# Kernel optimization log

Measured on AMD Instinct MI355X. Metric: run time of the kernel, lower is better.

## Reference

```python
import jax, jax.numpy as jnp
import numpy as np

D_MODEL = 512
N_HEADS = 8
HEAD_DIM = 64
INNER = N_HEADS * HEAD_DIM
PAD = 128  # flash-attention style tile padding used by the custom kernel


def setup_inputs() -> dict:
    key = jax.random.key(0)
    ks = jax.random.split(key, 5)
    B, S = 2, 2048
    scale = 0.02
    return {
        "hidden_states": jax.random.normal(ks[0], (B, S, D_MODEL), dtype=jnp.float32),
        "Wq": jax.random.normal(ks[1], (D_MODEL, INNER), dtype=jnp.float32) * scale,
        "Wk": jax.random.normal(ks[2], (D_MODEL, INNER), dtype=jnp.float32) * scale,
        "Wv": jax.random.normal(ks[3], (D_MODEL, INNER), dtype=jnp.float32) * scale,
        "Wo": jax.random.normal(ks[4], (INNER, D_MODEL), dtype=jnp.float32) * scale,
    }


def _padded_attention(q, k, v):
    """Emulates torch.ops.knl.fwd: pad seq to a multiple of PAD, run
    non-causal scaled dot-product attention masking padded keys, then
    slice back to the original length. q,k,v: [B, S, INNER]."""
    B, S, _ = q.shape
    pad_len = (-S) % PAD
    Sp = S + pad_len
    pad_cfg = ((0, 0), (0, pad_len), (0, 0))
    qp = jnp.pad(q, pad_cfg)
    kp = jnp.pad(k, pad_cfg)
    vp = jnp.pad(v, pad_cfg)
    # [B, H, Sp, hd]
    qh = qp.reshape(B, Sp, N_HEADS, HEAD_DIM).transpose(0, 2, 1, 3)
    kh = kp.reshape(B, Sp, N_HEADS, HEAD_DIM).transpose(0, 2, 1, 3)
    vh = vp.reshape(B, Sp, N_HEADS, HEAD_DIM).transpose(0, 2, 1, 3)
    scale = 1.0 / np.sqrt(HEAD_DIM).astype(np.float32)
    scores = jnp.einsum("bhqd,bhkd->bhqk", qh, kh) * scale  # [B,H,Sp,Sp]
    key_valid = jnp.arange(Sp) < S  # mask out padded keys
    scores = jnp.where(key_valid[None, None, None, :], scores, jnp.float32(-1e30))
    probs = jax.nn.softmax(scores, axis=-1)
    out = jnp.einsum("bhqk,bhkd->bhqd", probs, vh)  # [B,H,Sp,hd]
    out = out.transpose(0, 2, 1, 3).reshape(B, Sp, INNER)
    return out[:, :S, :]


def reference(hidden_states, Wq, Wk, Wv, Wo):
    q = hidden_states @ Wq
    k = hidden_states @ Wk
    v = hidden_states @ Wv
    attn = _padded_attention(q, k, v)
    return attn @ Wo
```

## Files before the change

kernel.cpp:

```cpp
#include <hip/hip_runtime.h>

using bf16 = __bf16;
using bf16x4 = __attribute__((ext_vector_type(4))) __bf16;
using bf16x8 = __attribute__((ext_vector_type(8))) __bf16;
using floatx4 = __attribute__((ext_vector_type(4))) float;
using half4 = __attribute__((ext_vector_type(4))) _Float16;
using half8 = __attribute__((ext_vector_type(8))) _Float16;

#define D_MODEL 512
#define S_LEN 2048
#define HD 64
#define NH 8
#define M_TOT 4096
#define RS 72
#define NSPLIT 4
#define KSPAN (S_LEN / NSPLIT)
#define QSCALE 0.18033688f

__device__ __forceinline__ bf16x8 ld8(const bf16* p) {
    return *reinterpret_cast<const bf16x8*>(p);
}
__device__ __forceinline__ void gl_lds16(const bf16* g, bf16* l) {
    __builtin_amdgcn_global_load_lds(
        (const __attribute__((address_space(1))) void*)g,
        (__attribute__((address_space(3))) void*)l, 16, 0, 0);
}

__global__ __launch_bounds__(256) void prep(const float* __restrict__ w0,
                                            const float* __restrict__ w1,
                                            const float* __restrict__ w2,
                                            const float* __restrict__ w3,
                                            const float* __restrict__ X,
                                            bf16* __restrict__ WT,
                                            bf16* __restrict__ Xb) {
    int z = blockIdx.z;
    if (z == 4) {
        int i = (blockIdx.x * 256 + threadIdx.x) * 8;
        float4 a = *reinterpret_cast<const float4*>(X + i);
        float4 b = *reinterpret_cast<const float4*>(X + i + 4);
        bf16x8 o;
        o[0] = (bf16)a.x; o[1] = (bf16)a.y; o[2] = (bf16)a.z; o[3] = (bf16)a.w;
        o[4] = (bf16)b.x; o[5] = (bf16)b.y; o[6] = (bf16)b.z; o[7] = (bf16)b.w;
        *reinterpret_cast<bf16x8*>(Xb + i) = o;
        return;
    }
    if (blockIdx.x >= 256) return;
    __shared__ float t[32][33];
    const float* in = z == 0 ? w0 : z == 1 ? w1 : z == 2 ? w2 : w3;
    bf16* o = WT + (size_t)z * D_MODEL * D_MODEL;
    int x = threadIdx.x & 31;
    int y = threadIdx.x >> 5;
    int k0 = (blockIdx.x & 15) * 32, n0 = (blockIdx.x >> 4) * 32;
    for (int r = y; r < 32; r += 8) t[r][x] = in[(size_t)(k0 + r) * D_MODEL + n0 + x];
    __syncthreads();
    for (int r = y; r < 32; r += 8) o[(size_t)(n0 + r) * D_MODEL + k0 + x] = (bf16)t[x][r];
}

__global__ __launch_bounds__(256) void gemm_qkvf(const bf16* __restrict__ X,
                                                 const bf16* __restrict__ WT,
                                                 bf16* __restrict__ qk,
                                                 bf16* __restrict__ VT) {
    __shared__ __align__(16) bf16 As[64 * 64];
    __shared__ __align__(16) bf16 Bs[64 * 64];
    int lane = threadIdx.x & 63, wave = threadIdx.x >> 6;
    int l15 = lane & 15, quad = lane >> 4;
    int m0 = blockIdx.x * 64;
    int n0 = blockIdx.y * 64;
    int z = n0 >> 9;
    int h = (n0 >> 6) & 7;
    int wm = (wave & 1) * 32, wn = (wave >> 1) * 32;
    float oscale = (z == 0) ? QSCALE : 1.0f;

    int sr = lane >> 3;
    int sc = (lane & 7) ^ sr;
    const bf16* gA = X  + (size_t)(m0 + wave * 16 + sr) * D_MODEL + sc * 8;
    const bf16* gB = WT + (size_t)(n0 + wave * 16 + sr) * D_MODEL + sc * 8;
    bf16* ldsA = &As[(wave * 16) * 64];
    bf16* ldsB = &Bs[(wave * 16) * 64];
    int rx = l15 & 7;

    floatx4 acc[2][2] = {};
    for (int k0 = 0; k0 < D_MODEL; k0 += 64) {
        __syncthreads();
        gl_lds16(gA + k0, ldsA);
        gl_lds16(gA + (size_t)8 * D_MODEL + k0, ldsA + 8 * 64);
        gl_lds16(gB + k0, ldsB);
        gl_lds16(gB + (size_t)8 * D_MODEL + k0, ldsB + 8 * 64);
        __syncthreads();
        bf16x8 af[2][2], bfr[2][2];
        #pragma unroll
        for (int mt = 0; mt < 2; mt++)
            #pragma unroll
            for (int kh = 0; kh < 2; kh++)
                af[mt][kh] = ld8(&As[(wm + mt * 16 + l15) * 64 + (((quad + 4 * kh) ^ rx)) * 8]);
        #pragma unroll
        for (int nt = 0; nt < 2; nt++)
            #pragma unroll
            for (int kh = 0; kh < 2; kh++)
                bfr[nt][kh] = ld8(&Bs[(wn + nt * 16 + l15) * 64 + (((quad + 4 * kh) ^ rx)) * 8]);
        #pragma unroll
        for (int mt = 0; mt < 2; mt++)
            #pragma unroll
            for (int nt = 0; nt < 2; nt++) {
                acc[mt][nt] = __builtin_amdgcn_mfma_f32_16x16x32_bf16(af[mt][0], bfr[nt][0], acc[mt][nt], 0, 0, 0);
                acc[mt][nt] = __builtin_amdgcn_mfma_f32_16x16x32_bf16(af[mt][1], bfr[nt][1], acc[mt][nt], 0, 0, 0);
            }
    }

    if (z < 2) {
        bf16* dst = qk + (size_t)z * M_TOT * HD * NH;
        #pragma unroll
        for (int mt = 0; mt < 2; mt++)
            #pragma unroll
            for (int nt = 0; nt < 2; nt++)
                #pragma unroll
                for (int r = 0; r < 4; r++) {
                    int m = m0 + wm + mt * 16 + quad * 4 + r;
                    int n = wn + nt * 16 + l15;
                    int b = m >> 11, s = m & 2047;
                    dst[((size_t)(b * NH + h) * S_LEN + s) * HD + n] = (bf16)(acc[mt][nt][r] * oscale);
                }
    } else {
        #pragma unroll
        for (int mt = 0; mt < 2; mt++)
            #pragma unroll
            for (int nt = 0; nt < 2; nt++) {
                int m = m0 + wm + mt * 16 + quad * 4;
                int d = wn + nt * 16 + l15;
                int b = m >> 11, s = m & 2047;
                bf16x4 pk;
                pk[0] = (bf16)acc[mt][nt][0]; pk[1] = (bf16)acc[mt][nt][1];
                pk[2] = (bf16)acc[mt][nt][2]; pk[3] = (bf16)acc[mt][nt][3];
                *reinterpret_cast<bf16x4*>(&VT[((size_t)(b * NH + h) * HD + d) * S_LEN + s]) = pk;
            }
    }
}

__global__ __launch_bounds__(256) void attn_split(const bf16* __restrict__ qg,
                                                  const bf16* __restrict__ kg,
                                                  const bf16* __restrict__ vt,
                                                  _Float16* __restrict__ Opart,
                                                  float* __restrict__ lsum) {
    __shared__ __align__(16) bf16 Kl[64 * 64];
    __shared__ __align__(16) bf16 Vl[64 * 64];
    __shared__ __align__(16) bf16 Pl[128 * RS];
    int tid = threadIdx.x;
    int lane = tid & 63, wave = tid >> 6;
    int l15 = lane & 15, quad = lane >> 4;
    int bh = blockIdx.y, split = blockIdx.z;
    int q0 = blockIdx.x * 128;
    const bf16* qb = qg + (size_t)bh * S_LEN * HD;
    const bf16* kb = kg + (size_t)bh * S_LEN * HD + (size_t)split * KSPAN * HD;
    const bf16* vb = vt + (size_t)bh * HD * S_LEN + split * KSPAN;

    int qA = q0 + wave * 32 + l15;
    int qB = qA + 16;
    bf16x8 qf[2][2];
    qf[0][0] = ld8(qb + (size_t)qA * HD + quad * 8);
    qf[0][1] = ld8(qb + (size_t)qA * HD + 32 + quad * 8);
    qf[1][0] = ld8(qb + (size_t)qB * HD + quad * 8);
    qf[1][1] = ld8(qb + (size_t)qB * HD + 32 + quad * 8);
    floatx4 O[2][4] = {};
    float l_i[2] = {0.f, 0.f};

    int sr = lane >> 3;
    int sc = (lane & 7) ^ sr;
    const bf16* gK = kb + (size_t)(wave * 16 + sr) * HD + sc * 8;
    const bf16* gV = vb + (size_t)(wave * 16 + sr) * S_LEN + sc * 8;
    bf16* ldsK = &Kl[(wave * 16) * 64];
    bf16* ldsV = &Vl[(wave * 16) * 64];
    int rx = l15 & 7;

    for (int kt = 0; kt < KSPAN; kt += 64) {
        __syncthreads();
        gl_lds16(gK + (size_t)kt * HD, ldsK);
        gl_lds16(gK + (size_t)(kt + 8) * HD, ldsK + 8 * 64);
        gl_lds16(gV + kt, ldsV);
        gl_lds16(gV + (size_t)8 * S_LEN + kt, ldsV + 8 * 64);
        __syncthreads();

        #pragma unroll
        for (int qh = 0; qh < 2; qh++) {
            floatx4 sc4[4];
            #pragma unroll
            for (int nt = 0; nt < 4; nt++) {
                floatx4 z = {};
                bf16x8 a0 = ld8(&Kl[(nt * 16 + l15) * 64 + (quad ^ rx) * 8]);
                bf16x8 a1 = ld8(&Kl[(nt * 16 + l15) * 64 + ((quad + 4) ^ rx) * 8]);
                z = __builtin_amdgcn_mfma_f32_16x16x32_bf16(a0, qf[qh][0], z, 0, 0, 0);
                z = __builtin_amdgcn_mfma_f32_16x16x32_bf16(a1, qf[qh][1], z, 0, 0, 0);
                sc4[nt] = z;
            }
            #pragma unroll
            for (int nt = 0; nt < 4; nt++) {
                bf16x4 pk;
                #pragma unroll
                for (int r = 0; r < 4; r++) {
                    float p = exp2f(sc4[nt][r]);
                    l_i[qh] += p;
                    pk[r] = (bf16)p;
                }
                *reinterpret_cast<bf16x4*>(
                    &Pl[(wave * 32 + qh * 16 + l15) * RS + nt * 16 + quad * 4]) = pk;
            }
        }
        __syncthreads();

        bf16x8 pb[2][2];
        #pragma unroll
        for (int qh = 0; qh < 2; qh++) {
            pb[qh][0] = ld8(&Pl[(wave * 32 + qh * 16 + l15) * RS + quad * 8]);
            pb[qh][1] = ld8(&Pl[(wave * 32 + qh * 16 + l15) * RS + 32 + quad * 8]);
        }
        #pragma unroll
        for (int nt = 0; nt < 4; nt++) {
            bf16x8 v0 = ld8(&Vl[(nt * 16 + l15) * 64 + (quad ^ rx) * 8]);
            bf16x8 v1 = ld8(&Vl[(nt * 16 + l15) * 64 + ((quad + 4) ^ rx) * 8]);
            #pragma unroll
            for (int qh = 0; qh < 2; qh++) {
                O[qh][nt] = __builtin_amdgcn_mfma_f32_16x16x32_bf16(v0, pb[qh][0], O[qh][nt], 0, 0, 0);
                O[qh][nt] = __builtin_amdgcn_mfma_f32_16x16x32_bf16(v1, pb[qh][1], O[qh][nt], 0, 0, 0);
            }
        }
    }

    #pragma unroll
    for (int qh = 0; qh < 2; qh++) {
        float l = l_i[qh];
        l += __shfl_xor(l, 16, 64);
        l += __shfl_xor(l, 32, 64);
        int q = (qh == 0) ? qA : qB;
        size_t obase = (((size_t)(split * 16 + bh)) * S_LEN + q) * HD;
        #pragma unroll
        for (int nt = 0; nt < 4; nt++) {
            half4 h;
            h[0] = (_Float16)O[qh][nt][0]; h[1] = (_Float16)O[qh][nt][1];
            h[2] = (_Float16)O[qh][nt][2]; h[3] = (_Float16)O[qh][nt][3];
            *reinterpret_cast<half4*>(&Opart[obase + nt * 16 + quad * 4]) = h;
        }
        if (quad == 0)
            lsum[((size_t)(split * 16 + bh)) * S_LEN + q] = l;
    }
}

__global__ __launch_bounds__(256) void gemm_outm(const _Float16* __restrict__ Opart,
                                                 const float* __restrict__ lsum,
                                                 const bf16* __restrict__ WoT,
                                                 float* __restrict__ out) {
    __shared__ __align__(16) bf16 As[64 * 64];
    __shared__ __align__(16) bf16 Bs[64 * 64];
    __shared__ float invl[64 * 8];
    int tid = threadIdx.x;
    int lane = tid & 63, wave = tid >> 6;
    int l15 = lane & 15, quad = lane >> 4;
    int m0 = blockIdx.x * 64;
    int n0 = blockIdx.y * 64;
    int wm = (wave & 1) * 32, wn = (wave >> 1) * 32;

    for (int i = tid; i < 512; i += 256) {
        int row = i >> 3, h = i & 7;
        int mm = m0 + row;
        int b = mm >> 11, q = mm & 2047;
        float l = 0.f;
        #pragma unroll
        for (int s = 0; s < NSPLIT; s++)
            l += lsum[((size_t)(s * 16 + b * NH + h)) * S_LEN + q];
        invl[i] = 1.f / l;
    }

    int sr = lane >> 3;
    int sc = (lane & 7) ^ sr;
    const bf16* gB = WoT + (size_t)(n0 + wave * 16 + sr) * D_MODEL + sc * 8;
    bf16* ldsA = &As[(wave * 16) * 64];
    bf16* ldsB = &Bs[(wave * 16) * 64];
    int rx = l15 & 7;

    floatx4 acc[2][2] = {};
    for (int k0 = 0; k0 < D_MODEL; k0 += 64) {
        __syncthreads();
        gl_lds16(gB + k0, ldsB);
        gl_lds16(gB + (size_t)8 * D_MODEL + k0, ldsB + 8 * 64);
        int h = k0 >> 6;
        #pragma unroll
        for (int st = 0; st < 2; st++) {
            int row = wave * 16 + sr + st * 8;
            int mm = m0 + row;
            int b = mm >> 11, q = mm & 2047;
            float iv = invl[row * 8 + h];
            float a8[8] = {};
            #pragma unroll
            for (int s = 0; s < NSPLIT; s++) {
                half8 hp = *reinterpret_cast<const half8*>(
                    &Opart[(((size_t)(s * 16 + b * NH + h)) * S_LEN + q) * HD + sc * 8]);
                #pragma unroll
                for (int j = 0; j < 8; j++) a8[j] += (float)hp[j];
            }
            bf16x8 v;
            #pragma unroll
            for (int j = 0; j < 8; j++) v[j] = (bf16)(a8[j] * iv);
            *reinterpret_cast<bf16x8*>(ldsA + st * 512 + lane * 8) = v;
        }
        __syncthreads();
        bf16x8 af[2][2], bfr[2][2];
        #pragma unroll
        for (int mt = 0; mt < 2; mt++)
            #pragma unroll
            for (int kh = 0; kh < 2; kh++)
                af[mt][kh] = ld8(&As[(wm + mt * 16 + l15) * 64 + (((quad + 4 * kh) ^ rx)) * 8]);
        #pragma unroll
        for (int nt = 0; nt < 2; nt++)
            #pragma unroll
            for (int kh = 0; kh < 2; kh++)
                bfr[nt][kh] = ld8(&Bs[(wn + nt * 16 + l15) * 64 + (((quad + 4 * kh) ^ rx)) * 8]);
        #pragma unroll
        for (int mt = 0; mt < 2; mt++)
            #pragma unroll
            for (int nt = 0; nt < 2; nt++) {
                acc[mt][nt] = __builtin_amdgcn_mfma_f32_16x16x32_bf16(af[mt][0], bfr[nt][0], acc[mt][nt], 0, 0, 0);
                acc[mt][nt] = __builtin_amdgcn_mfma_f32_16x16x32_bf16(af[mt][1], bfr[nt][1], acc[mt][nt], 0, 0, 0);
            }
    }

    #pragma unroll
    for (int mt = 0; mt < 2; mt++)
        #pragma unroll
        for (int nt = 0; nt < 2; nt++)
            #pragma unroll
            for (int r = 0; r < 4; r++) {
                int m = m0 + wm + mt * 16 + quad * 4 + r;
                int n = n0 + wn + nt * 16 + l15;
                out[(size_t)m * D_MODEL + n] = acc[mt][nt][r];
            }
}

extern "C" void kernel_launch(void* const* d_in, const int* in_sizes, int n_in,
                              void* d_out, int out_size, void* d_ws, size_t ws_size,
                              hipStream_t stream) {
    const float* X  = (const float*)d_in[0];
    const float* Wq = (const float*)d_in[1];
    const float* Wk = (const float*)d_in[2];
    const float* Wv = (const float*)d_in[3];
    const float* Wo = (const float*)d_in[4];
    float* out = (float*)d_out;
    bf16* ws  = (bf16*)d_ws;

    bf16* Xb  = ws;
    bf16* WT  = Xb + (size_t)M_TOT * D_MODEL;
    bf16* qk  = WT + (size_t)4 * D_MODEL * D_MODEL;
    bf16* VT  = qk + (size_t)2 * M_TOT * D_MODEL;
    _Float16* Opart = (_Float16*)(VT + (size_t)M_TOT * D_MODEL);
    float* lbuf = (float*)(Opart + (size_t)NSPLIT * 16 * S_LEN * HD);

    prep<<<dim3(1024, 1, 5), 256, 0, stream>>>(Wq, Wk, Wv, Wo, X, WT, Xb);
    gemm_qkvf<<<dim3(64, 24), 256, 0, stream>>>(Xb, WT, qk, VT);
    attn_split<<<dim3(16, 16, NSPLIT), 256, 0, stream>>>(qk,
                                                         qk + (size_t)M_TOT * D_MODEL,
                                                         VT, Opart, lbuf);
    gemm_outm<<<dim3(64, 8), 256, 0, stream>>>(Opart, lbuf,
                                               WT + (size_t)3 * D_MODEL * D_MODEL, out);
}
```

Measured before the change: 132.7 us.

## Pass attention probabilities via lane shuffles instead of LDS, halve query tile

The P matrix is no longer written to a shared-memory staging buffer and read back after a barrier. It is rearranged from the score accumulator layout into the MFMA operand layout with cross-lane shuffles and selects. Each block now handles 64 queries, one 16-row tile per wave, and the grid doubles. The launch bound asks for higher occupancy. This removes an LDS round-trip and a __syncthreads per tile, but it halves K/V reuse per block, so K/V tiles are loaded twice as often, and it adds many shuffle instructions.

```diff
diff --git a/kernel.cpp b/kernel.cpp
--- a/kernel.cpp
+++ b/kernel.cpp
@@ -12,7 +12,6 @@
 #define HD 64
 #define NH 8
 #define M_TOT 4096
-#define RS 72
 #define NSPLIT 4
 #define KSPAN (S_LEN / NSPLIT)
 #define QSCALE 0.18033688f
@@ -136,32 +135,26 @@
     }
 }
 
-__global__ __launch_bounds__(256) void attn_split(const bf16* __restrict__ qg,
-                                                  const bf16* __restrict__ kg,
-                                                  const bf16* __restrict__ vt,
-                                                  _Float16* __restrict__ Opart,
-                                                  float* __restrict__ lsum) {
+__global__ __launch_bounds__(256, 8) void attn_split(const bf16* __restrict__ qg,
+                                                     const bf16* __restrict__ kg,
+                                                     const bf16* __restrict__ vt,
+                                                     _Float16* __restrict__ Opart,
+                                                     float* __restrict__ lsum) {
     __shared__ __align__(16) bf16 Kl[64 * 64];
     __shared__ __align__(16) bf16 Vl[64 * 64];
-    __shared__ __align__(16) bf16 Pl[128 * RS];
     int tid = threadIdx.x;
     int lane = tid & 63, wave = tid >> 6;
     int l15 = lane & 15, quad = lane >> 4;
     int bh = blockIdx.y, split = blockIdx.z;
-    int q0 = blockIdx.x * 128;
+    int q0 = blockIdx.x * 64;
     const bf16* qb = qg + (size_t)bh * S_LEN * HD;
     const bf16* kb = kg + (size_t)bh * S_LEN * HD + (size_t)split * KSPAN * HD;
     const bf16* vb = vt + (size_t)bh * HD * S_LEN + split * KSPAN;
-
-    int qA = q0 + wave * 32 + l15;
-    int qB = qA + 16;
-    bf16x8 qf[2][2];
-    qf[0][0] = ld8(qb + (size_t)qA * HD + quad * 8);
-    qf[0][1] = ld8(qb + (size_t)qA * HD + 32 + quad * 8);
-    qf[1][0] = ld8(qb + (size_t)qB * HD + quad * 8);
-    qf[1][1] = ld8(qb + (size_t)qB * HD + 32 + quad * 8);
-    floatx4 O[2][4] = {};
-    float l_i[2] = {0.f, 0.f};
+    int q = q0 + wave * 16 + l15;
+    bf16x8 qf0 = ld8(qb + (size_t)q * HD + quad * 8);
+    bf16x8 qf1 = ld8(qb + (size_t)q * HD + 32 + quad * 8);
+    floatx4 O[4] = {};
+    float l_i = 0.f;
 
     int sr = lane >> 3;
     int sc = (lane & 7) ^ sr;
@@ -170,6 +163,9 @@
     bf16* ldsK = &Kl[(wave * 16) * 64];
     bf16* ldsV = &Vl[(wave * 16) * 64];
     int rx = l15 & 7;
+    int sa = ((quad & 1) << 5) + l15;
+    int sb = sa + 16;
+    bool himux = (quad & 2) != 0;
 
     for (int kt = 0; kt < KSPAN; kt += 64) {
         __syncthreads();
@@ -179,68 +175,71 @@
         gl_lds16(gV + (size_t)8 * S_LEN + kt, ldsV + 8 * 64);
         __syncthreads();
 
-        #pragma unroll
-        for (int qh = 0; qh < 2; qh++) {
-            floatx4 sc4[4];
-            #pragma unroll
-            for (int nt = 0; nt < 4; nt++) {
-                floatx4 z = {};
-                bf16x8 a0 = ld8(&Kl[(nt * 16 + l15) * 64 + (quad ^ rx) * 8]);
-                bf16x8 a1 = ld8(&Kl[(nt * 16 + l15) * 64 + ((quad + 4) ^ rx) * 8]);
-                z = __builtin_amdgcn_mfma_f32_16x16x32_bf16(a0, qf[qh][0], z, 0, 0, 0);
-                z = __builtin_amdgcn_mfma_f32_16x16x32_bf16(a1, qf[qh][1], z, 0, 0, 0);
-                sc4[nt] = z;
-            }
-            #pragma unroll
-            for (int nt = 0; nt < 4; nt++) {
-                bf16x4 pk;
-                #pragma unroll
-                for (int r = 0; r < 4; r++) {
-                    float p = exp2f(sc4[nt][r]);
-                    l_i[qh] += p;
-                    pk[r] = (bf16)p;
-                }
-                *reinterpret_cast<bf16x4*>(
-                    &Pl[(wave * 32 + qh * 16 + l15) * RS + nt * 16 + quad * 4]) = pk;
-            }
-        }
-        __syncthreads();
-
-        bf16x8 pb[2][2];
-        #pragma unroll
-        for (int qh = 0; qh < 2; qh++) {
-            pb[qh][0] = ld8(&Pl[(wave * 32 + qh * 16 + l15) * RS + quad * 8]);
-            pb[qh][1] = ld8(&Pl[(wave * 32 + qh * 16 + l15) * RS + 32 + quad * 8]);
-        }
+        floatx4 sc4[4];
+        #pragma unroll
+        for (int nt = 0; nt < 4; nt++) {
+            floatx4 z = {};
+            bf16x8 a0 = ld8(&Kl[(nt * 16 + l15) * 64 + (quad ^ rx) * 8]);
+            bf16x8 a1 = ld8(&Kl[(nt * 16 + l15) * 64 + ((quad + 4) ^ rx) * 8]);
+            z = __builtin_amdgcn_mfma_f32_16x16x32_bf16(a0, qf0, z, 0, 0, 0);
+            z = __builtin_amdgcn_mfma_f32_16x16x32_bf16(a1, qf1, z, 0, 0, 0);
+            sc4[nt] = z;
+        }
+
+        int2 pq[4];
+        #pragma unroll
+        for (int nt = 0; nt < 4; nt++) {
+            bf16x4 pk;
+            #pragma unroll
+            for (int r = 0; r < 4; r++) {
+                float p = exp2f(sc4[nt][r]);
+                l_i += p;
+                pk[r] = (bf16)p;
+            }
+            pq[nt] = __builtin_bit_cast(int2, pk);
+        }
+
+        bf16x8 pb[2];
+        #pragma unroll
+        for (int h2 = 0; h2 < 2; h2++) {
+            int t0 = __shfl(pq[2 * h2].x,     sa, 64);
+            int t1 = __shfl(pq[2 * h2].y,     sa, 64);
+            int t2 = __shfl(pq[2 * h2 + 1].x, sa, 64);
+            int t3 = __shfl(pq[2 * h2 + 1].y, sa, 64);
+            int u0 = __shfl(pq[2 * h2].x,     sb, 64);
+            int u1 = __shfl(pq[2 * h2].y,     sb, 64);
+            int u2 = __shfl(pq[2 * h2 + 1].x, sb, 64);
+            int u3 = __shfl(pq[2 * h2 + 1].y, sb, 64);
+            int4 v;
+            v.x = himux ? t2 : t0;
+            v.y = himux ? t3 : t1;
+            v.z = himux ? u2 : u0;
+            v.w = himux ? u3 : u1;
+            pb[h2] = __builtin_bit_cast(bf16x8, v);
+        }
+
         #pragma unroll
         for (int nt = 0; nt < 4; nt++) {
             bf16x8 v0 = ld8(&Vl[(nt * 16 + l15) * 64 + (quad ^ rx) * 8]);
             bf16x8 v1 = ld8(&Vl[(nt * 16 + l15) * 64 + ((quad + 4) ^ rx) * 8]);
-            #pragma unroll
-            for (int qh = 0; qh < 2; qh++) {
-                O[qh][nt] = __builtin_amdgcn_mfma_f32_16x16x32_bf16(v0, pb[qh][0], O[qh][nt], 0, 0, 0);
-                O[qh][nt] = __builtin_amdgcn_mfma_f32_16x16x32_bf16(v1, pb[qh][1], O[qh][nt], 0, 0, 0);
-            }
-        }
-    }
-
+            O[nt] = __builtin_amdgcn_mfma_f32_16x16x32_bf16(v0, pb[0], O[nt], 0, 0, 0);
+            O[nt] = __builtin_amdgcn_mfma_f32_16x16x32_bf16(v1, pb[1], O[nt], 0, 0, 0);
+        }
+    }
+
+    l_i += __shfl_xor(l_i, 16, 64);
+    l_i += __shfl_xor(l_i, 32, 64);
+
+    size_t obase = (((size_t)(split * 16 + bh)) * S_LEN + q) * HD;
     #pragma unroll
-    for (int qh = 0; qh < 2; qh++) {
-        float l = l_i[qh];
-        l += __shfl_xor(l, 16, 64);
-        l += __shfl_xor(l, 32, 64);
-        int q = (qh == 0) ? qA : qB;
-        size_t obase = (((size_t)(split * 16 + bh)) * S_LEN + q) * HD;
-        #pragma unroll
-        for (int nt = 0; nt < 4; nt++) {
-            half4 h;
-            h[0] = (_Float16)O[qh][nt][0]; h[1] = (_Float16)O[qh][nt][1];
-            h[2] = (_Float16)O[qh][nt][2]; h[3] = (_Float16)O[qh][nt][3];
-            *reinterpret_cast<half4*>(&Opart[obase + nt * 16 + quad * 4]) = h;
-        }
-        if (quad == 0)
-            lsum[((size_t)(split * 16 + bh)) * S_LEN + q] = l;
-    }
+    for (int nt = 0; nt < 4; nt++) {
+        half4 hv;
+        hv[0] = (_Float16)O[nt][0]; hv[1] = (_Float16)O[nt][1];
+        hv[2] = (_Float16)O[nt][2]; hv[3] = (_Float16)O[nt][3];
+        *reinterpret_cast<half4*>(&Opart[obase + nt * 16 + quad * 4]) = hv;
+    }
+    if (quad == 0)
+        lsum[((size_t)(split * 16 + bh)) * S_LEN + q] = l_i;
 }
 
 __global__ __launch_bounds__(256) void gemm_outm(const _Float16* __restrict__ Opart,
@@ -353,7 +352,7 @@
 
     prep<<<dim3(1024, 1, 5), 256, 0, stream>>>(Wq, Wk, Wv, Wo, X, WT, Xb);
     gemm_qkvf<<<dim3(64, 24), 256, 0, stream>>>(Xb, WT, qk, VT);
-    attn_split<<<dim3(16, 16, NSPLIT), 256, 0, stream>>>(qk,
+    attn_split<<<dim3(32, 16, NSPLIT), 256, 0, stream>>>(qk,
                                                          qk + (size_t)M_TOT * D_MODEL,
                                                          VT, Opart, lbuf);
     gemm_outm<<<dim3(64, 8), 256, 0, stream>>>(Opart, lbuf,
```

Result: no change. 130.7 us (-1.5%).

## Redistribute attention probabilities via wave shuffles instead of LDS round-trip

Applied to the files above, without the earlier changes.

Removes the P staging buffer in shared memory and its block-wide barrier. Probabilities are now moved from the score MFMA output layout into the PV MFMA operand layout with cross-lane shuffles inside each wave. The QK loop is also restructured so each K fragment load serves both query halves, and launch bounds request four blocks per CU. This trades LDS traffic and a __syncthreads for many ds_bpermute-style shuffles and extra register pressure.

```diff
diff --git a/kernel.cpp b/kernel.cpp
--- a/kernel.cpp
+++ b/kernel.cpp
@@ -12,7 +12,6 @@
 #define HD 64
 #define NH 8
 #define M_TOT 4096
-#define RS 72
 #define NSPLIT 4
 #define KSPAN (S_LEN / NSPLIT)
 #define QSCALE 0.18033688f
@@ -136,14 +135,13 @@
     }
 }
 
-__global__ __launch_bounds__(256) void attn_split(const bf16* __restrict__ qg,
-                                                  const bf16* __restrict__ kg,
-                                                  const bf16* __restrict__ vt,
-                                                  _Float16* __restrict__ Opart,
-                                                  float* __restrict__ lsum) {
+__global__ __launch_bounds__(256, 4) void attn_split(const bf16* __restrict__ qg,
+                                                     const bf16* __restrict__ kg,
+                                                     const bf16* __restrict__ vt,
+                                                     _Float16* __restrict__ Opart,
+                                                     float* __restrict__ lsum) {
     __shared__ __align__(16) bf16 Kl[64 * 64];
     __shared__ __align__(16) bf16 Vl[64 * 64];
-    __shared__ __align__(16) bf16 Pl[128 * RS];
     int tid = threadIdx.x;
     int lane = tid & 63, wave = tid >> 6;
     int l15 = lane & 15, quad = lane >> 4;
@@ -152,7 +150,6 @@
     const bf16* qb = qg + (size_t)bh * S_LEN * HD;
     const bf16* kb = kg + (size_t)bh * S_LEN * HD + (size_t)split * KSPAN * HD;
     const bf16* vb = vt + (size_t)bh * HD * S_LEN + split * KSPAN;
-
     int qA = q0 + wave * 32 + l15;
     int qB = qA + 16;
     bf16x8 qf[2][2];
@@ -170,6 +167,9 @@
     bf16* ldsK = &Kl[(wave * 16) * 64];
     bf16* ldsV = &Vl[(wave * 16) * 64];
     int rx = l15 & 7;
+    int sa = ((quad & 1) << 5) + l15;
+    int sb = sa + 16;
+    bool himux = (quad & 2) != 0;
 
     for (int kt = 0; kt < KSPAN; kt += 64) {
         __syncthreads();
@@ -179,39 +179,54 @@
         gl_lds16(gV + (size_t)8 * S_LEN + kt, ldsV + 8 * 64);
         __syncthreads();
 
+        floatx4 sc4[2][4];
+        #pragma unroll
+        for (int nt = 0; nt < 4; nt++) {
+            bf16x8 a0 = ld8(&Kl[(nt * 16 + l15) * 64 + (quad ^ rx) * 8]);
+            bf16x8 a1 = ld8(&Kl[(nt * 16 + l15) * 64 + ((quad + 4) ^ rx) * 8]);
+            floatx4 z0 = {}, z1 = {};
+            z0 = __builtin_amdgcn_mfma_f32_16x16x32_bf16(a0, qf[0][0], z0, 0, 0, 0);
+            z0 = __builtin_amdgcn_mfma_f32_16x16x32_bf16(a1, qf[0][1], z0, 0, 0, 0);
+            z1 = __builtin_amdgcn_mfma_f32_16x16x32_bf16(a0, qf[1][0], z1, 0, 0, 0);
+            z1 = __builtin_amdgcn_mfma_f32_16x16x32_bf16(a1, qf[1][1], z1, 0, 0, 0);
+            sc4[0][nt] = z0;
+            sc4[1][nt] = z1;
+        }
+
+        bf16x8 pb[2][2];
         #pragma unroll
         for (int qh = 0; qh < 2; qh++) {
-            floatx4 sc4[4];
-            #pragma unroll
-            for (int nt = 0; nt < 4; nt++) {
-                floatx4 z = {};
-                bf16x8 a0 = ld8(&Kl[(nt * 16 + l15) * 64 + (quad ^ rx) * 8]);
-                bf16x8 a1 = ld8(&Kl[(nt * 16 + l15) * 64 + ((quad + 4) ^ rx) * 8]);
-                z = __builtin_amdgcn_mfma_f32_16x16x32_bf16(a0, qf[qh][0], z, 0, 0, 0);
-                z = __builtin_amdgcn_mfma_f32_16x16x32_bf16(a1, qf[qh][1], z, 0, 0, 0);
-                sc4[nt] = z;
-            }
+            int2 pq[4];
             #pragma unroll
             for (int nt = 0; nt < 4; nt++) {
                 bf16x4 pk;
                 #pragma unroll
                 for (int r = 0; r < 4; r++) {
-                    float p = exp2f(sc4[nt][r]);
+                    float p = exp2f(sc4[qh][nt][r]);
                     l_i[qh] += p;
                     pk[r] = (bf16)p;
                 }
-                *reinterpret_cast<bf16x4*>(
-                    &Pl[(wave * 32 + qh * 16 + l15) * RS + nt * 16 + quad * 4]) = pk;
-            }
-        }
-        __syncthreads();
-
-        bf16x8 pb[2][2];
-        #pragma unroll
-        for (int qh = 0; qh < 2; qh++) {
-            pb[qh][0] = ld8(&Pl[(wave * 32 + qh * 16 + l15) * RS + quad * 8]);
-            pb[qh][1] = ld8(&Pl[(wave * 32 + qh * 16 + l15) * RS + 32 + quad * 8]);
-        }
+                pq[nt] = __builtin_bit_cast(int2, pk);
+            }
+            #pragma unroll
+            for (int h2 = 0; h2 < 2; h2++) {
+                int t0 = __shfl(pq[2 * h2].x,     sa, 64);
+                int t1 = __shfl(pq[2 * h2].y,     sa, 64);
+                int t2 = __shfl(pq[2 * h2 + 1].x, sa, 64);
+                int t3 = __shfl(pq[2 * h2 + 1].y, sa, 64);
+                int u0 = __shfl(pq[2 * h2].x,     sb, 64);
+                int u1 = __shfl(pq[2 * h2].y,     sb, 64);
+                int u2 = __shfl(pq[2 * h2 + 1].x, sb, 64);
+                int u3 = __shfl(pq[2 * h2 + 1].y, sb, 64);
+                int4 v;
+                v.x = himux ? t2 : t0;
+                v.y = himux ? t3 : t1;
+                v.z = himux ? u2 : u0;
+                v.w = himux ? u3 : u1;
+                pb[qh][h2] = __builtin_bit_cast(bf16x8, v);
+            }
+        }
+
         #pragma unroll
         for (int nt = 0; nt < 4; nt++) {
             bf16x8 v0 = ld8(&Vl[(nt * 16 + l15) * 64 + (quad ^ rx) * 8]);
@@ -233,10 +248,10 @@
         size_t obase = (((size_t)(split * 16 + bh)) * S_LEN + q) * HD;
         #pragma unroll
         for (int nt = 0; nt < 4; nt++) {
-            half4 h;
-            h[0] = (_Float16)O[qh][nt][0]; h[1] = (_Float16)O[qh][nt][1];
-            h[2] = (_Float16)O[qh][nt][2]; h[3] = (_Float16)O[qh][nt][3];
-            *reinterpret_cast<half4*>(&Opart[obase + nt * 16 + quad * 4]) = h;
+            half4 hv;
+            hv[0] = (_Float16)O[qh][nt][0]; hv[1] = (_Float16)O[qh][nt][1];
+            hv[2] = (_Float16)O[qh][nt][2]; hv[3] = (_Float16)O[qh][nt][3];
+            *reinterpret_cast<half4*>(&Opart[obase + nt * 16 + quad * 4]) = hv;
         }
         if (quad == 0)
             lsum[((size_t)(split * 16 + bh)) * S_LEN + q] = l;
```

Result: no change. 133.0 us (+0.3%).
